# Optimization experiments

Hardware: AMD Instinct MI355X
Metric: run time of the kernel (lower is better)

The kernel has to match this reference:

```python
import jax, jax.numpy as jnp
import numpy as np
import math

EMB, SEQ, OUT, FF, B = 1024, 1024, 2, 1024, 32
EPS = 1e-5


def _build_pe(seq_len, emb_dim):
    # Faithful to the buggy torch loop: for even i, pe[pos,i] is first set to sin
    # then immediately overwritten by cos(pos / 10000**(2*(i+1)/emb_dim));
    # odd indices are never written (stay 0).
    pos = np.arange(seq_len, dtype=np.float64)[:, None]
    i = np.arange(0, emb_dim, 2, dtype=np.float64)[None, :]
    pe = np.zeros((seq_len, emb_dim), dtype=np.float32)
    pe[:, ::2] = np.cos(pos / 10000.0 ** (2.0 * (i + 1.0) / emb_dim)).astype(np.float32)
    return jnp.asarray(pe)[None]  # [1, S, D]


def setup_inputs() -> dict:
    key = jax.random.key(0)
    ks = jax.random.split(key, 24)
    std = 0.02
    W = lambda k, o, i: jax.random.normal(k, (o, i), jnp.float32) * std
    b = lambda k, o: jax.random.normal(k, (o,), jnp.float32) * std
    return {
        "x": jax.random.normal(ks[0], (B, SEQ, EMB), jnp.float32),
        "pe": _build_pe(SEQ, EMB),
        "ln1_g": jnp.ones((EMB,), jnp.float32), "ln1_b": jnp.zeros((EMB,), jnp.float32),
        "Wq": W(ks[1], EMB, EMB), "bq": b(ks[2], EMB),
        "Wk": W(ks[3], EMB, EMB), "bk": b(ks[4], EMB),
        "Wv": W(ks[5], EMB, EMB), "bv": b(ks[6], EMB),
        "Wo": W(ks[7], EMB, EMB), "bo": b(ks[8], EMB),
        "ln2_g": jnp.ones((EMB,), jnp.float32), "ln2_b": jnp.zeros((EMB,), jnp.float32),
        "W1": W(ks[9], FF, EMB), "b1": b(ks[10], FF),
        "W2": W(ks[11], EMB, FF), "b2": b(ks[12], EMB),
        "Wc": W(ks[13], OUT, EMB), "bc": b(ks[14], OUT),
    }


def _ln(x, g, bias):
    mu = jnp.mean(x, axis=-1, keepdims=True)
    var = jnp.mean(jnp.square(x - mu), axis=-1, keepdims=True)
    return (x - mu) * jax.lax.rsqrt(var + EPS) * g + bias


def _block(x, ln1_g, ln1_b, Wq, bq, Wk, bk, Wv, bv, Wo, bo, ln2_g, ln2_b, W1, b1, W2, b2):
    h = _ln(x, ln1_g, ln1_b)
    q = h @ Wq.T + bq
    k = h @ Wk.T + bk
    v = h @ Wv.T + bv
    scores = jnp.einsum('bqd,bkd->bqk', q, k) / math.sqrt(EMB)
    w = jax.nn.softmax(scores, axis=-1)  # [B,S,S]
    attn = jnp.einsum('bqk,bkd->bqd', w, v) @ Wo.T + bo
    x2 = x + attn  # dropout is identity in eval
    h2 = _ln(x2, ln2_g, ln2_b)
    ff = jax.nn.relu(h2 @ W1.T + b1) @ W2.T + b2
    return x2 + ff, w


def reference(x, pe, ln1_g, ln1_b, Wq, bq, Wk, bk, Wv, bv, Wo, bo, ln2_g, ln2_b, W1, b1, W2, b2, Wc, bc):
    x1 = math.sqrt(EMB) * x + pe
    # Original forward applies block net2_1 twice (net2_2 is unused) -> reuse params.
    p = (ln1_g, ln1_b, Wq, bq, Wk, bk, Wv, bv, Wo, bo, ln2_g, ln2_b, W1, b1, W2, b2)
    x2_1, w1 = _block(x1, *p)
    x2_2, w2 = _block(x2_1, *p)
    logits = x2_2[:, 0, :] @ Wc.T + bc
    return logits, w1, w2
```

## Files before the change

kernel.cpp:

```cpp
#include <hip/hip_runtime.h>
#include <cstdint>


#define AS1 __attribute__((address_space(1)))
#define AS3 __attribute__((address_space(3)))

typedef __attribute__((ext_vector_type(8))) short bf16x8;
typedef __attribute__((ext_vector_type(4))) float f32x4;
typedef __attribute__((ext_vector_type(4))) unsigned short us4;
typedef __attribute__((ext_vector_type(8))) unsigned short us8;

__device__ __forceinline__ unsigned short f2bf(float f) {
  unsigned int u = __builtin_bit_cast(unsigned int, f);
  u += 0x7fffu + ((u >> 16) & 1u);
  return (unsigned short)(u >> 16);
}
__device__ __forceinline__ float bf2f(unsigned short h) {
  return __builtin_bit_cast(float, (unsigned int)h << 16);
}

__device__ __forceinline__ void gload_lds16(const void* g, void* l) {
  auto gp = reinterpret_cast<AS1 unsigned int*>(reinterpret_cast<uintptr_t>(g));
  auto lp = reinterpret_cast<AS3 unsigned int*>(reinterpret_cast<uintptr_t>(l));
  __builtin_amdgcn_global_load_lds(gp, lp, 16, 0, 0);
}

enum { M_BF16 = 0, M_RELU = 1, M_QKV = 2, M_SCBF = 3, M_RESID = 4 };

#define MFMA_QUAD(qi, qj)                                                          \
  do {                                                                             \
    _Pragma("unroll") for (int i2 = 0; i2 < 4; ++i2) {                             \
      _Pragma("unroll") for (int j2 = 0; j2 < 2; ++j2) {                           \
        f32x4& c = acc[(qi) * 4 + i2][(qj) * 2 + j2];                              \
        c = __builtin_amdgcn_mfma_f32_16x16x32_bf16(aF[(qi) * 4 + i2][0],          \
                                                    bF[(qj) * 2 + j2][0], c, 0, 0, 0); \
        c = __builtin_amdgcn_mfma_f32_16x16x32_bf16(aF[(qi) * 4 + i2][1],          \
                                                    bF[(qj) * 2 + j2][1], c, 0, 0, 0); \
      }                                                                            \
    }                                                                              \
  } while (0)

template<int MODE>
__global__ __launch_bounds__(512, 2) void gemm_bt(
    const unsigned short* __restrict__ A, long long sAb,
    const unsigned short* __restrict__ B, long long sBb,
    const float* __restrict__ bias,
    const float* __restrict__ resid,
    float* __restrict__ outF,
    unsigned short* __restrict__ outBF,
    long long sOb, int N, int K, float scale)
{
  __shared__ __align__(16) unsigned short lds[65536];
  const int t    = threadIdx.x;
  const int w    = t >> 6;
  const int lane = t & 63;
  const int quad = lane >> 4;
  const int l16  = lane & 15;
  const int l7   = l16 & 7;
  const int wm   = w >> 2;
  const int wn   = w & 3;
  const int bz   = blockIdx.z;
  const unsigned short* Ab = A + (long long)bz * sAb;
  const unsigned short* Bb = B + (long long)bz * sBb;
  const int m0 = blockIdx.y * 256;
  const int n0 = blockIdx.x * 256;

  const int sr8  = lane >> 3;
  const int gseg = ((lane & 7) ^ sr8) << 3;
  const unsigned short* aSrc = Ab + (long long)(m0 + w * 8 + sr8) * K + gseg;
  const unsigned short* bSrc = Bb + (long long)(n0 + w * 8 + sr8) * K + gseg;
  const int ldsW = w << 9;

  const int aOff = (wm * 128 + l16) * 64;
  const int bOff = 16384 + (wn * 64 + l16) * 64;
  const int seg0 = (quad ^ l7) << 3;
  const int seg1 = ((quad + 4) ^ l7) << 3;

  const int NG = K >> 6;

  const f32x4 zero = {0.f, 0.f, 0.f, 0.f};
  f32x4 acc[8][4];
#pragma unroll
  for (int i = 0; i < 8; ++i)
#pragma unroll
    for (int j = 0; j < 4; ++j) acc[i][j] = zero;

  bf16x8 aF[8][2];
  bf16x8 bF[4][2];

#define STAGE_A(kt, h, SL) do {                                                    \
    const unsigned short* _s = aSrc + (long long)(h) * 128 * K + (kt) * 64;        \
    unsigned short* _d = &lds[(SL) + ((h) << 13) + ldsW];                          \
    gload_lds16(_s, _d);                                                           \
    gload_lds16(_s + 64 * (long long)K, _d + 4096);                                \
  } while (0)
#define STAGE_B(kt, h, SL) do {                                                    \
    const unsigned short* _s = bSrc + (long long)(h) * 128 * K + (kt) * 64;        \
    unsigned short* _d = &lds[(SL) + 16384 + ((h) << 13) + ldsW];                  \
    gload_lds16(_s, _d);                                                           \
    gload_lds16(_s + 64 * (long long)K, _d + 4096);                                \
  } while (0)

#define READ_A03(SL)                                                               \
    _Pragma("unroll") for (int i2 = 0; i2 < 4; ++i2) {                             \
      aF[i2][0] = *(const bf16x8*)&lds[(SL) + aOff + i2 * 1024 + seg0];            \
      aF[i2][1] = *(const bf16x8*)&lds[(SL) + aOff + i2 * 1024 + seg1];            \
    }
#define READ_A47(SL)                                                               \
    _Pragma("unroll") for (int i2 = 0; i2 < 4; ++i2) {                             \
      aF[4 + i2][0] = *(const bf16x8*)&lds[(SL) + aOff + (4 + i2) * 1024 + seg0];  \
      aF[4 + i2][1] = *(const bf16x8*)&lds[(SL) + aOff + (4 + i2) * 1024 + seg1];  \
    }
#define READ_B01(SL)                                                               \
    _Pragma("unroll") for (int j2 = 0; j2 < 2; ++j2) {                             \
      bF[j2][0] = *(const bf16x8*)&lds[(SL) + bOff + j2 * 1024 + seg0];            \
      bF[j2][1] = *(const bf16x8*)&lds[(SL) + bOff + j2 * 1024 + seg1];            \
    }
#define READ_B23(SL)                                                               \
    _Pragma("unroll") for (int j2 = 0; j2 < 2; ++j2) {                             \
      bF[2 + j2][0] = *(const bf16x8*)&lds[(SL) + bOff + (2 + j2) * 1024 + seg0];  \
      bF[2 + j2][1] = *(const bf16x8*)&lds[(SL) + bOff + (2 + j2) * 1024 + seg1];  \
    }

#define KTILE(g, CUR, OTH)                                                         \
  {                                                                        \
    READ_A03(CUR)                                                                  \
    READ_B01(CUR)                                                                  \
    if ((g) + 1 < NG) STAGE_B((g) + 1, 1, OTH);                                    \
    __builtin_amdgcn_s_barrier();                                                  \
    asm volatile("s_waitcnt lgkmcnt(0)" ::: "memory");                             \
    __builtin_amdgcn_s_setprio(1);                                                 \
    MFMA_QUAD(0, 0);                                                               \
    __builtin_amdgcn_s_setprio(0);                                                 \
    __builtin_amdgcn_s_barrier();                                                  \
  }                                                                                \
  {                                                                        \
    READ_A47(CUR)                                                                  \
    __builtin_amdgcn_s_barrier();                                                  \
    asm volatile("s_waitcnt lgkmcnt(0)" ::: "memory");                             \
    __builtin_amdgcn_s_setprio(1);                                                 \
    MFMA_QUAD(1, 0);                                                               \
    __builtin_amdgcn_s_setprio(0);                                                 \
    __builtin_amdgcn_s_barrier();                                                  \
  }                                                                                \
  {                                                                        \
    READ_B23(CUR)                                                                  \
    if ((g) + 2 < NG) STAGE_A((g) + 2, 0, CUR);                                    \
    __builtin_amdgcn_s_barrier();                                                  \
    asm volatile("s_waitcnt lgkmcnt(0)" ::: "memory");                             \
    __builtin_amdgcn_s_setprio(1);                                                 \
    MFMA_QUAD(1, 1);                                                               \
    __builtin_amdgcn_s_setprio(0);                                                 \
    __builtin_amdgcn_s_barrier();                                                  \
  }                                                                                \
  {                                                                        \
    if ((g) + 2 < NG) { STAGE_A((g) + 2, 1, CUR); STAGE_B((g) + 2, 0, CUR); }      \
    if ((g) + 2 < NG) {                                                            \
      asm volatile("s_waitcnt vmcnt(6)" ::: "memory");                             \
    } else {                                                                       \
      asm volatile("s_waitcnt vmcnt(0)" ::: "memory");                             \
    }                                                                              \
    __builtin_amdgcn_s_barrier();                                                  \
    __builtin_amdgcn_s_setprio(1);                                                 \
    MFMA_QUAD(0, 1);                                                               \
    __builtin_amdgcn_s_setprio(0);                                                 \
    __builtin_amdgcn_s_barrier();                                                  \
  }

  STAGE_A(0, 0, 0); STAGE_A(0, 1, 0); STAGE_B(0, 0, 0); STAGE_B(0, 1, 0);
  STAGE_A(1, 0, 32768); STAGE_A(1, 1, 32768); STAGE_B(1, 0, 32768);
  asm volatile("s_waitcnt vmcnt(6)" ::: "memory");
  __builtin_amdgcn_s_barrier();

#pragma unroll 1
  for (int g = 0; g < NG; g += 2) {
    KTILE(g, 0, 32768)
    KTILE(g + 1, 32768, 0)
  }

#undef KTILE
#undef STAGE_A
#undef STAGE_B

  const int segq = (MODE == M_QKV) ? (n0 >> 10) : 0;
  if (MODE == M_RESID) {
#pragma unroll
    for (int i = 0; i < 8; ++i) {
      const int mt = m0 + wm * 128 + i * 16 + quad * 4;
#pragma unroll
      for (int j = 0; j < 4; ++j) {
        const int nt = n0 + wn * 64 + j * 16 + l16;
        const float bv = bias[nt];
        f32x4 d = acc[i][j];
#pragma unroll
        for (int r = 0; r < 4; ++r) {
          const long long idx = (long long)(mt + r) * N + nt;
          outF[idx] = resid[idx] + d[r] + bv;
        }
      }
    }
  } else {
#pragma unroll
    for (int i = 0; i < 8; ++i) {
      const int lr0 = wm * 128 + i * 16 + quad * 4;
#pragma unroll
      for (int j = 0; j < 4; ++j) {
        const int colg = wn * 64 + j * 16 + l16;
        float bv = 0.0f;
        if (MODE == M_BF16 || MODE == M_RELU || MODE == M_QKV)
          bv = bias ? bias[n0 + colg] : 0.0f;
        f32x4 d = acc[i][j];
#pragma unroll
        for (int r = 0; r < 4; ++r) {
          float v;
          if (MODE == M_SCBF) v = d[r] * scale;
          else                v = d[r] + bv;
          if (MODE == M_RELU) v = fmaxf(v, 0.0f);
          const int lr = lr0 + r;
          lds[lr * 256 + (colg ^ ((lr & 7) << 3))] = f2bf(v);
        }
      }
    }
    __syncthreads();
    if (MODE == M_QKV && segq == 2) {
      const int dl = t & 255;
      const int sh = t >> 8;
      unsigned short* dst = outBF + 2LL * 33554432LL
                          + (long long)(m0 >> 10) * 1048576
                          + (long long)((n0 & 1023) + dl) * 1024 + (m0 & 1023);
#pragma unroll
      for (int k = 0; k < 16; ++k) {
        const int s0 = sh * 128 + k * 8;
        us8 vv;
#pragma unroll
        for (int i = 0; i < 8; ++i)
          vv[i] = lds[(s0 + i) * 256 + (dl ^ (((s0 + i) & 7) << 3))];
        *(us8*)&dst[s0] = vv;
      }
    } else {
#pragma unroll
      for (int k = 0; k < 16; ++k) {
        const int lr = k * 16 + (t >> 5);
        const int colg = (t & 31) * 8;
        us8 vv = *(const us8*)&lds[lr * 256 + (colg ^ ((lr & 7) << 3))];
        if (MODE == M_QKV) {
          unsigned short* dst = outBF + (long long)segq * 33554432LL;
          *(us8*)&dst[(long long)(m0 + lr) * 1024 + (n0 - (segq << 10)) + colg] = vv;
        } else {
          *(us8*)&outBF[(long long)bz * sOb + (long long)(m0 + lr) * N + (n0 + colg)] = vv;
        }
      }
    }
  }
}

template<int EMBED>
__global__ __launch_bounds__(256) void ln_kernel(
    const float* __restrict__ xin, const float* __restrict__ pe,
    float* __restrict__ x1out,
    const float* __restrict__ g, const float* __restrict__ bb,
    unsigned short* __restrict__ hout)
{
  __shared__ float red[8];
  const long long row = blockIdx.x;
  const int t = threadIdx.x, lane = t & 63, w = t >> 6;
  float4 v = *(const float4*)(xin + row * 1024 + t * 4);
  if (EMBED) {
    const int s = (int)(row & 1023);
    float4 p = *(const float4*)(pe + (long long)s * 1024 + t * 4);
    v.x = 32.0f * v.x + p.x;
    v.y = 32.0f * v.y + p.y;
    v.z = 32.0f * v.z + p.z;
    v.w = 32.0f * v.w + p.w;
    *(float4*)(x1out + row * 1024 + t * 4) = v;
  }
  float sum = v.x + v.y + v.z + v.w;
  float sq  = v.x * v.x + v.y * v.y + v.z * v.z + v.w * v.w;
#pragma unroll
  for (int off = 32; off > 0; off >>= 1) {
    sum += __shfl_down(sum, off, 64);
    sq  += __shfl_down(sq,  off, 64);
  }
  if (lane == 0) { red[w] = sum; red[4 + w] = sq; }
  __syncthreads();
  sum = red[0] + red[1] + red[2] + red[3];
  sq  = red[4] + red[5] + red[6] + red[7];
  const float mu  = sum * (1.0f / 1024.0f);
  const float var = sq * (1.0f / 1024.0f) - mu * mu;
  const float rs  = rsqrtf(var + 1e-5f);
  float4 gg = *(const float4*)(g + t * 4);
  float4 bv = *(const float4*)(bb + t * 4);
  us4 h;
  h[0] = f2bf((v.x - mu) * rs * gg.x + bv.x);
  h[1] = f2bf((v.y - mu) * rs * gg.y + bv.y);
  h[2] = f2bf((v.z - mu) * rs * gg.z + bv.z);
  h[3] = f2bf((v.w - mu) * rs * gg.w + bv.w);
  *(us4*)(hout + row * 1024 + t * 4) = h;
}

__global__ __launch_bounds__(256) void softmax_kernel(
    const unsigned short* __restrict__ sbf,
    float* __restrict__ wout, unsigned short* __restrict__ wbf)
{
  __shared__ float red[8];
  const long long row = blockIdx.x;
  const int t = threadIdx.x, lane = t & 63, w = t >> 6;
  us4 sv = *(const us4*)(sbf + row * 1024 + t * 4);
  float4 v;
  v.x = bf2f(sv[0]); v.y = bf2f(sv[1]); v.z = bf2f(sv[2]); v.w = bf2f(sv[3]);
  float mx = fmaxf(fmaxf(v.x, v.y), fmaxf(v.z, v.w));
#pragma unroll
  for (int off = 32; off > 0; off >>= 1) mx = fmaxf(mx, __shfl_down(mx, off, 64));
  if (lane == 0) red[w] = mx;
  __syncthreads();
  mx = fmaxf(fmaxf(red[0], red[1]), fmaxf(red[2], red[3]));
  __syncthreads();
  const float e0 = __expf(v.x - mx), e1 = __expf(v.y - mx);
  const float e2 = __expf(v.z - mx), e3 = __expf(v.w - mx);
  float s = e0 + e1 + e2 + e3;
#pragma unroll
  for (int off = 32; off > 0; off >>= 1) s += __shfl_down(s, off, 64);
  if (lane == 0) red[w] = s;
  __syncthreads();
  s = red[0] + red[1] + red[2] + red[3];
  const float inv = 1.0f / s;
  float4 o; o.x = e0 * inv; o.y = e1 * inv; o.z = e2 * inv; o.w = e3 * inv;
  *(float4*)(wout + row * 1024 + t * 4) = o;
  us4 ob;
  ob[0] = f2bf(o.x); ob[1] = f2bf(o.y); ob[2] = f2bf(o.z); ob[3] = f2bf(o.w);
  *(us4*)(wbf + row * 1024 + t * 4) = ob;
}

__global__ __launch_bounds__(256) void prep_kernel(
    const float* __restrict__ Wq, const float* __restrict__ Wk, const float* __restrict__ Wv,
    const float* __restrict__ Wo, const float* __restrict__ W1, const float* __restrict__ W2,
    const float* __restrict__ bq, const float* __restrict__ bk, const float* __restrict__ bv,
    unsigned short* __restrict__ qkvw, unsigned short* __restrict__ Wo_bf,
    unsigned short* __restrict__ W1_bf, unsigned short* __restrict__ W2_bf,
    float* __restrict__ qkvb)
{
  const int y = blockIdx.y;
  const long long i = blockIdx.x * 256 + threadIdx.x;
  if (y == 6) {
    if (i < 768) {
      const float* src = (i < 256) ? bq : (i < 512) ? bk : bv;
      float4 v = *(const float4*)(src + (i & 255) * 4);
      *(float4*)(qkvb + i * 4) = v;
    }
    return;
  }
  const float* src;
  unsigned short* dst;
  switch (y) {
    case 0: src = Wq; dst = qkvw;            break;
    case 1: src = Wk; dst = qkvw + 1048576;  break;
    case 2: src = Wv; dst = qkvw + 2097152;  break;
    case 3: src = Wo; dst = Wo_bf;           break;
    case 4: src = W1; dst = W1_bf;           break;
    default: src = W2; dst = W2_bf;          break;
  }
  float4 v = *(const float4*)(src + i * 4);
  us4 o;
  o[0] = f2bf(v.x); o[1] = f2bf(v.y); o[2] = f2bf(v.z); o[3] = f2bf(v.w);
  *(us4*)(dst + i * 4) = o;
}

__global__ __launch_bounds__(256) void logits_kernel(
    const float* __restrict__ x, const float* __restrict__ Wc,
    const float* __restrict__ bc, float* __restrict__ out)
{
  __shared__ float red[4];
  const int blk = blockIdx.x;
  const int b = blk >> 1, o = blk & 1;
  const int t = threadIdx.x, lane = t & 63, w = t >> 6;
  const float* xr = x + (long long)b * 1048576;
  const float* wr = Wc + o * 1024;
  float4 xv = *(const float4*)(xr + t * 4);
  float4 wv = *(const float4*)(wr + t * 4);
  float s = xv.x * wv.x + xv.y * wv.y + xv.z * wv.z + xv.w * wv.w;
#pragma unroll
  for (int off = 32; off > 0; off >>= 1) s += __shfl_down(s, off, 64);
  if (lane == 0) red[w] = s;
  __syncthreads();
  if (t == 0) out[blk] = red[0] + red[1] + red[2] + red[3] + bc[o];
}

extern "C" void kernel_launch(void* const* d_in, const int* in_sizes, int n_in,
                              void* d_out, int out_size, void* d_ws, size_t ws_size,
                              hipStream_t stream)
{
  const float* x    = (const float*)d_in[0];
  const float* pe   = (const float*)d_in[1];
  const float* ln1g = (const float*)d_in[2];
  const float* ln1b = (const float*)d_in[3];
  const float* Wq   = (const float*)d_in[4];
  const float* bq   = (const float*)d_in[5];
  const float* Wk   = (const float*)d_in[6];
  const float* bk   = (const float*)d_in[7];
  const float* Wv   = (const float*)d_in[8];
  const float* bv   = (const float*)d_in[9];
  const float* Wo   = (const float*)d_in[10];
  const float* bo   = (const float*)d_in[11];
  const float* ln2g = (const float*)d_in[12];
  const float* ln2b = (const float*)d_in[13];
  const float* W1   = (const float*)d_in[14];
  const float* b1   = (const float*)d_in[15];
  const float* W2   = (const float*)d_in[16];
  const float* b2   = (const float*)d_in[17];
  const float* Wc   = (const float*)d_in[18];
  const float* bc   = (const float*)d_in[19];
  float* out = (float*)d_out;

  char* ws = (char*)d_ws;
  float*          xbuf  = (float*)ws;
  unsigned short* h_bf  = (unsigned short*)(ws + 134217728LL);
  unsigned short* q_bf  = (unsigned short*)(ws + 134217728LL + 1 * 67108864LL);
  unsigned short* k_bf  = (unsigned short*)(ws + 134217728LL + 2 * 67108864LL);
  unsigned short* vT_bf = (unsigned short*)(ws + 134217728LL + 3 * 67108864LL);
  unsigned short* wts   = (unsigned short*)(ws + 134217728LL + 4 * 67108864LL);
  unsigned short* QKV_bf = wts;
  unsigned short* Wo_bf  = wts + 3LL * 1048576;
  unsigned short* W1_bf  = wts + 4LL * 1048576;
  unsigned short* W2_bf  = wts + 5LL * 1048576;
  float*          qkvb   = (float*)(wts + 6LL * 1048576);
  unsigned short* sc_bf   = h_bf;
  unsigned short* w_bf    = k_bf;
  unsigned short* attn_bf = q_bf;
  unsigned short* ff1_bf  = vT_bf;

  const dim3 blk(256);
  const dim3 blkG(512);
  prep_kernel<<<dim3(1024, 7), blk, 0, stream>>>(Wq, Wk, Wv, Wo, W1, W2, bq, bk, bv,
                                                 QKV_bf, Wo_bf, W1_bf, W2_bf, qkvb);

  const dim3 gQKV(12, 128, 1);
  const dim3 gProj(4, 128, 1);
  const dim3 gAttn(4, 4, 32);

  for (int blkI = 0; blkI < 2; ++blkI) {
    float* wslot = out + 64 + (long long)blkI * 33554432LL;

    if (blkI == 0)
      ln_kernel<1><<<32768, blk, 0, stream>>>(x, pe, xbuf, ln1g, ln1b, h_bf);
    else
      ln_kernel<0><<<32768, blk, 0, stream>>>(xbuf, nullptr, nullptr, ln1g, ln1b, h_bf);

    gemm_bt<M_QKV><<<gQKV, blkG, 0, stream>>>(h_bf, 0, QKV_bf, 0, qkvb, nullptr,
                                              nullptr, q_bf, 0, 3072, 1024, 1.0f);

    gemm_bt<M_SCBF><<<gAttn, blkG, 0, stream>>>(q_bf, 1048576, k_bf, 1048576, nullptr,
                                                nullptr, nullptr, sc_bf, 1048576,
                                                1024, 1024, 0.03125f);
    softmax_kernel<<<32768, blk, 0, stream>>>(sc_bf, wslot, w_bf);

    gemm_bt<M_BF16><<<gAttn, blkG, 0, stream>>>(w_bf, 1048576, vT_bf, 1048576, nullptr,
                                                nullptr, nullptr, attn_bf, 1048576,
                                                1024, 1024, 1.0f);
    gemm_bt<M_RESID><<<gProj, blkG, 0, stream>>>(attn_bf, 0, Wo_bf, 0, bo, xbuf,
                                                 xbuf, nullptr, 0, 1024, 1024, 1.0f);

    ln_kernel<0><<<32768, blk, 0, stream>>>(xbuf, nullptr, nullptr, ln2g, ln2b, h_bf);
    gemm_bt<M_RELU><<<gProj, blkG, 0, stream>>>(h_bf, 0, W1_bf, 0, b1, nullptr,
                                                nullptr, ff1_bf, 0, 1024, 1024, 1.0f);
    gemm_bt<M_RESID><<<gProj, blkG, 0, stream>>>(ff1_bf, 0, W2_bf, 0, b2, xbuf,
                                                 xbuf, nullptr, 0, 1024, 1024, 1.0f);
  }

  logits_kernel<<<64, blk, 0, stream>>>(xbuf, Wc, bc, out);
  (void)in_sizes; (void)n_in; (void)out_size; (void)ws_size;
}
```

Measured before the change: 2.153 ms.

## Remap workgroups across XCDs, rebalance B staging, write GEMM epilogue directly

Workgroup IDs are remapped so that consecutive tiles land on the same XCD (an 8-way interleave), aiming for better L2 reuse of shared A and B panels. The global-to-LDS staging of the next B half-tile is split across two sub-phases, and the vmcnt waits are reduced to match. The LDS-staged, vectorised bf16 epilogue is replaced with direct per-element global stores. That removes a __syncthreads and the LDS round-trip but produces narrower, less coalesced writes.

Result: slower. 2.325 ms (+8.0%).

```diff
diff --git a/kernel.cpp b/kernel.cpp
--- a/kernel.cpp
+++ b/kernel.cpp
@@ -8,7 +8,6 @@
 typedef __attribute__((ext_vector_type(8))) short bf16x8;
 typedef __attribute__((ext_vector_type(4))) float f32x4;
 typedef __attribute__((ext_vector_type(4))) unsigned short us4;
-typedef __attribute__((ext_vector_type(8))) unsigned short us8;
 
 __device__ __forceinline__ unsigned short f2bf(float f) {
   unsigned int u = __builtin_bit_cast(unsigned int, f);
@@ -59,11 +58,20 @@
   const int l7   = l16 & 7;
   const int wm   = w >> 2;
   const int wn   = w & 3;
-  const int bz   = blockIdx.z;
+
+  const int gx = gridDim.x, gy = gridDim.y;
+  const int nwg = gx * gy * (int)gridDim.z;
+  int lid = (int)blockIdx.x + gx * ((int)blockIdx.y + gy * (int)blockIdx.z);
+  if ((nwg & 7) == 0) lid = (lid & 7) * (nwg >> 3) + (lid >> 3);
+  const int bx = lid % gx;
+  const int t1 = lid / gx;
+  const int by = t1 % gy;
+  const int bz = t1 / gy;
+
   const unsigned short* Ab = A + (long long)bz * sAb;
   const unsigned short* Bb = B + (long long)bz * sBb;
-  const int m0 = blockIdx.y * 256;
-  const int n0 = blockIdx.x * 256;
+  const int m0 = by * 256;
+  const int n0 = bx * 256;
 
   const int sr8  = lane >> 3;
   const int gseg = ((lane & 7) ^ sr8) << 3;
@@ -126,7 +134,7 @@
   {                                                                        \
     READ_A03(CUR)                                                                  \
     READ_B01(CUR)                                                                  \
-    if ((g) + 1 < NG) STAGE_B((g) + 1, 1, OTH);                                    \
+    if ((g) + 1 < NG) STAGE_B((g) + 1, 0, OTH);                                    \
     __builtin_amdgcn_s_barrier();                                                  \
     asm volatile("s_waitcnt lgkmcnt(0)" ::: "memory");                             \
     __builtin_amdgcn_s_setprio(1);                                                 \
@@ -136,6 +144,7 @@
   }                                                                                \
   {                                                                        \
     READ_A47(CUR)                                                                  \
+    if ((g) + 1 < NG) STAGE_B((g) + 1, 1, OTH);                                    \
     __builtin_amdgcn_s_barrier();                                                  \
     asm volatile("s_waitcnt lgkmcnt(0)" ::: "memory");                             \
     __builtin_amdgcn_s_setprio(1);                                                 \
@@ -154,9 +163,9 @@
     __builtin_amdgcn_s_barrier();                                                  \
   }                                                                                \
   {                                                                        \
-    if ((g) + 2 < NG) { STAGE_A((g) + 2, 1, CUR); STAGE_B((g) + 2, 0, CUR); }      \
+    if ((g) + 2 < NG) STAGE_A((g) + 2, 1, CUR);                                    \
     if ((g) + 2 < NG) {                                                            \
-      asm volatile("s_waitcnt vmcnt(6)" ::: "memory");                             \
+      asm volatile("s_waitcnt vmcnt(4)" ::: "memory");                             \
     } else {                                                                       \
       asm volatile("s_waitcnt vmcnt(0)" ::: "memory");                             \
     }                                                                              \
@@ -168,8 +177,8 @@
   }
 
   STAGE_A(0, 0, 0); STAGE_A(0, 1, 0); STAGE_B(0, 0, 0); STAGE_B(0, 1, 0);
-  STAGE_A(1, 0, 32768); STAGE_A(1, 1, 32768); STAGE_B(1, 0, 32768);
-  asm volatile("s_waitcnt vmcnt(6)" ::: "memory");
+  STAGE_A(1, 0, 32768); STAGE_A(1, 1, 32768);
+  asm volatile("s_waitcnt vmcnt(4)" ::: "memory");
   __builtin_amdgcn_s_barrier();
 
 #pragma unroll 1
@@ -182,72 +191,49 @@
 #undef STAGE_A
 #undef STAGE_B
 
-  const int segq = (MODE == M_QKV) ? (n0 >> 10) : 0;
-  if (MODE == M_RESID) {
-#pragma unroll
-    for (int i = 0; i < 8; ++i) {
-      const int mt = m0 + wm * 128 + i * 16 + quad * 4;
-#pragma unroll
-      for (int j = 0; j < 4; ++j) {
-        const int nt = n0 + wn * 64 + j * 16 + l16;
+#pragma unroll
+  for (int i = 0; i < 8; ++i) {
+    const int mt = m0 + wm * 128 + i * 16 + quad * 4;
+#pragma unroll
+    for (int j = 0; j < 4; ++j) {
+      const int nt = n0 + wn * 64 + j * 16 + l16;
+      f32x4 d = acc[i][j];
+      if (MODE == M_BF16 || MODE == M_RELU) {
+        const float bv = bias ? bias[nt] : 0.0f;
+#pragma unroll
+        for (int r = 0; r < 4; ++r) {
+          float v = d[r] + bv;
+          if (MODE == M_RELU) v = fmaxf(v, 0.0f);
+          outBF[(long long)bz * sOb + (long long)(mt + r) * N + nt] = f2bf(v);
+        }
+      } else if (MODE == M_SCBF) {
+#pragma unroll
+        for (int r = 0; r < 4; ++r)
+          outBF[(long long)bz * sOb + (long long)(mt + r) * N + nt] = f2bf(d[r] * scale);
+      } else if (MODE == M_RESID) {
         const float bv = bias[nt];
-        f32x4 d = acc[i][j];
 #pragma unroll
         for (int r = 0; r < 4; ++r) {
           const long long idx = (long long)(mt + r) * N + nt;
           outF[idx] = resid[idx] + d[r] + bv;
         }
-      }
-    }
-  } else {
-#pragma unroll
-    for (int i = 0; i < 8; ++i) {
-      const int lr0 = wm * 128 + i * 16 + quad * 4;
-#pragma unroll
-      for (int j = 0; j < 4; ++j) {
-        const int colg = wn * 64 + j * 16 + l16;
-        float bv = 0.0f;
-        if (MODE == M_BF16 || MODE == M_RELU || MODE == M_QKV)
-          bv = bias ? bias[n0 + colg] : 0.0f;
-        f32x4 d = acc[i][j];
-#pragma unroll
-        for (int r = 0; r < 4; ++r) {
-          float v;
-          if (MODE == M_SCBF) v = d[r] * scale;
-          else                v = d[r] + bv;
-          if (MODE == M_RELU) v = fmaxf(v, 0.0f);
-          const int lr = lr0 + r;
-          lds[lr * 256 + (colg ^ ((lr & 7) << 3))] = f2bf(v);
-        }
-      }
-    }
-    __syncthreads();
-    if (MODE == M_QKV && segq == 2) {
-      const int dl = t & 255;
-      const int sh = t >> 8;
-      unsigned short* dst = outBF + 2LL * 33554432LL
-                          + (long long)(m0 >> 10) * 1048576
-                          + (long long)((n0 & 1023) + dl) * 1024 + (m0 & 1023);
-#pragma unroll
-      for (int k = 0; k < 16; ++k) {
-        const int s0 = sh * 128 + k * 8;
-        us8 vv;
-#pragma unroll
-        for (int i = 0; i < 8; ++i)
-          vv[i] = lds[(s0 + i) * 256 + (dl ^ (((s0 + i) & 7) << 3))];
-        *(us8*)&dst[s0] = vv;
-      }
-    } else {
-#pragma unroll
-      for (int k = 0; k < 16; ++k) {
-        const int lr = k * 16 + (t >> 5);
-        const int colg = (t & 31) * 8;
-        us8 vv = *(const us8*)&lds[lr * 256 + (colg ^ ((lr & 7) << 3))];
-        if (MODE == M_QKV) {
-          unsigned short* dst = outBF + (long long)segq * 33554432LL;
-          *(us8*)&dst[(long long)(m0 + lr) * 1024 + (n0 - (segq << 10)) + colg] = vv;
+      } else if (MODE == M_QKV) {
+        const int seg = n0 >> 10;
+        const int ntl = nt - (seg << 10);
+        const float bv = bias[nt];
+        if (seg < 2) {
+          unsigned short* dst = outBF + (long long)seg * 33554432LL;
+#pragma unroll
+          for (int r = 0; r < 4; ++r)
+            dst[(long long)(mt + r) * 1024 + ntl] = f2bf(d[r] + bv);
         } else {
-          *(us8*)&outBF[(long long)bz * sOb + (long long)(m0 + lr) * N + (n0 + colg)] = vv;
+          unsigned short* dst = outBF + 2LL * 33554432LL;
+          us4 pk;
+#pragma unroll
+          for (int r = 0; r < 4; ++r) pk[r] = f2bf(d[r] + bv);
+          const int b = mt >> 10;
+          const int s = mt & 1023;
+          *(us4*)&dst[(long long)b * 1048576 + (long long)ntl * 1024 + s] = pk;
         }
       }
     }
```
